# Kernel optimization log

Measured on AMD Instinct MI355X. Metric: run time of the kernel, lower is better.

The kernel has to match this reference:

```python
import jax, jax.numpy as jnp
import numpy as np

B, N, D_IN, D_OUT = 8, 2048, 512, 512


def setup_inputs() -> dict:
    key = jax.random.key(0)
    ks = jax.random.split(key, 9)
    s = 1.0 / np.sqrt(D_IN)
    return {
        "x": jax.random.normal(ks[0], (B, N, D_IN), dtype=jnp.float32),
        "adj": jax.random.uniform(ks[1], (B, N, N), dtype=jnp.float32, maxval=3.0),
        "Wq": jax.random.uniform(ks[2], (D_IN, D_OUT), jnp.float32, -s, s),
        "bq": jax.random.uniform(ks[3], (D_OUT,), jnp.float32, -s, s),
        "Wk": jax.random.uniform(ks[4], (D_IN, D_OUT), jnp.float32, -s, s),
        "bk": jax.random.uniform(ks[5], (D_OUT,), jnp.float32, -s, s),
        "Wv": jax.random.uniform(ks[6], (D_IN, D_OUT), jnp.float32, -s, s),
        "bv": jax.random.uniform(ks[7], (D_OUT,), jnp.float32, -s, s),
        "scale": jnp.float32(1.0),
        "width": jnp.float32(2.0),
    }


def reference(x, adj, Wq, bq, Wk, bk, Wv, bv, scale, width):
    # Linear projections
    Q = jnp.einsum("bnd,de->bne", x, Wq) + bq
    K = jnp.einsum("bnd,de->bne", x, Wk) + bk
    V = jnp.einsum("bnd,de->bne", x, Wv) + bv
    inv_sqrt_d = 1.0 / jnp.sqrt(jnp.float32(D_OUT))
    scores = jnp.einsum("bqe,bke->bqk", Q, K) * inv_sqrt_d  # [B,N,N]
    # Learned Gaussian distance mask, multiplicatively fused into scores
    masks = jnp.exp(-((adj - scale) ** 2 / width))
    attn = jax.nn.softmax(scores * masks, axis=-1)
    return jnp.einsum("bqk,bke->bqe", attn, V)
```

## Files before the change

### kernel.cpp

```cpp
#include <hip/hip_runtime.h>
#include <hip/hip_bf16.h>
#include <cstdint>

typedef __attribute__((ext_vector_type(4))) float f32x4;
typedef __attribute__((ext_vector_type(8))) short s16x8;

#define LOG2E 1.44269504088896340736f

#define WAITV0 asm volatile("s_waitcnt vmcnt(0)" ::: "memory")
#define WAITV2 asm volatile("s_waitcnt vmcnt(2)" ::: "memory")
#define WAITV18 asm volatile("s_waitcnt vmcnt(18)" ::: "memory")
#define WAITLG asm volatile("s_waitcnt lgkmcnt(0)" ::: "memory")
#define COMPILER_FENCE asm volatile("" ::: "memory")

__device__ __forceinline__ unsigned short f2bf(float f) {
    unsigned int u = __builtin_bit_cast(unsigned int, f);
    u += 0x7FFFu + ((u >> 16) & 1u);
    return (unsigned short)(u >> 16);
}
__device__ __forceinline__ float bf2f(unsigned short u) {
    return __builtin_bit_cast(float, (unsigned int)u << 16);
}
__device__ __forceinline__ void gload_lds16(const void* g, void* l) {
    __builtin_amdgcn_global_load_lds(
        (const __attribute__((address_space(1))) unsigned int*)g,
        (__attribute__((address_space(3))) unsigned int*)l, 16, 0, 0);
}
__device__ __forceinline__ int m3(int v) {
    if (v >= 9) v -= 9;
    if (v >= 6) v -= 6;
    if (v >= 3) v -= 3;
    return v;
}


__global__ void convert_x_kernel(const float* __restrict__ x,
                                 unsigned short* __restrict__ xb, int n4) {
    int i = blockIdx.x * blockDim.x + threadIdx.x;
    if (i < n4) {
        const float4 v = reinterpret_cast<const float4*>(x)[i];
        ushort4 o;
        o.x = f2bf(v.x); o.y = f2bf(v.y); o.z = f2bf(v.z); o.w = f2bf(v.w);
        reinterpret_cast<ushort4*>(xb)[i] = o;
    }
}

__global__ void transpose_w_kernel(const float* __restrict__ Wq,
                                   const float* __restrict__ Wk,
                                   const float* __restrict__ Wv,
                                   unsigned short* __restrict__ WT) {
    int i = blockIdx.x * blockDim.x + threadIdx.x;
    int m = i >> 18;
    int r = i & 262143;
    int n = r & 511;
    int k = r >> 9;
    const float* W = (m == 0) ? Wq : (m == 1) ? Wk : Wv;
    WT[(m << 18) + n * 512 + k] = f2bf(W[k * 512 + n]);
}

__global__ __launch_bounds__(256, 2) void proj_gemm_kernel(
    const unsigned short* __restrict__ xb,
    const unsigned short* __restrict__ WT,
    const float* __restrict__ bq, const float* __restrict__ bk, const float* __restrict__ bv,
    unsigned short* __restrict__ Qb, unsigned short* __restrict__ Kb,
    unsigned short* __restrict__ VT)
{
    const int z = blockIdx.z;
    const unsigned short* Wt = WT + (z << 18);
    const float* bias = (z == 0) ? bq : (z == 1) ? bk : bv;

    const int gm = blockIdx.x * 128;
    const int gn = blockIdx.y * 128;
    const int wave = threadIdx.x >> 6, lane = threadIdx.x & 63;
    const int wr = wave >> 1, wc = wave & 1;
    const int lr = lane & 15, lg = lane >> 4;
    const int row0 = gm + wr * 64;
    const int col0 = gn + wc * 64;

    f32x4 acc[4][4];
    #pragma unroll
    for (int mi = 0; mi < 4; mi++)
        #pragma unroll
        for (int ni = 0; ni < 4; ni++)
            acc[mi][ni] = (f32x4){0.f, 0.f, 0.f, 0.f};

    for (int k0 = 0; k0 < 512; k0 += 32) {
        s16x8 a[4], b[4];
        #pragma unroll
        for (int mi = 0; mi < 4; mi++)
            a[mi] = *reinterpret_cast<const s16x8*>(xb + (size_t)(row0 + mi * 16 + lr) * 512 + k0 + lg * 8);
        #pragma unroll
        for (int ni = 0; ni < 4; ni++)
            b[ni] = *reinterpret_cast<const s16x8*>(Wt + (size_t)(col0 + ni * 16 + lr) * 512 + k0 + lg * 8);
        #pragma unroll
        for (int mi = 0; mi < 4; mi++)
            #pragma unroll
            for (int ni = 0; ni < 4; ni++)
                acc[mi][ni] = __builtin_amdgcn_mfma_f32_16x16x32_bf16(a[mi], b[ni], acc[mi][ni], 0, 0, 0);
    }

    #pragma unroll
    for (int ni = 0; ni < 4; ni++) {
        const int col = col0 + ni * 16 + lr;
        const float bs = bias[col];
        #pragma unroll
        for (int mi = 0; mi < 4; mi++) {
            const int rowb = row0 + mi * 16 + lg * 4;
            if (z == 2) {
                unsigned short h[4];
                #pragma unroll
                for (int j = 0; j < 4; j++) h[j] = f2bf(acc[mi][ni][j] + bs);
                const int bb = rowb >> 11;
                const int nn = rowb & 2047;
                ushort4 o; o.x = h[0]; o.y = h[1]; o.z = h[2]; o.w = h[3];
                *reinterpret_cast<ushort4*>(VT + (size_t)bb * (512 * 2048) + (size_t)col * 2048 + nn) = o;
            } else {
                unsigned short* dst = (z == 0) ? Qb : Kb;
                #pragma unroll
                for (int j = 0; j < 4; j++)
                    dst[(size_t)(rowb + j) * 512 + col] = f2bf(acc[mi][ni][j] + bs);
            }
        }
    }
}

__global__ __launch_bounds__(512, 2) void attn_kernel(
    const unsigned short* __restrict__ Qb,
    const unsigned short* __restrict__ Kb,
    const unsigned short* __restrict__ VTb,
    const float* __restrict__ adj,
    const float* __restrict__ scale_p, const float* __restrict__ width_p,
    unsigned short* __restrict__ Op,
    float* __restrict__ Mp, float* __restrict__ Lp)
{
    const int bid = blockIdx.x;
    const int x8 = bid & 7, jj = bid >> 3;
    const int bk = x8 + 8 * (jj >> 5);
    const int qt = jj & 31;
    const int b    = bk >> 1;
    const int kvh  = bk & 1;
    const int wave = threadIdx.x >> 6;
    const int lane = threadIdx.x & 63;
    const int lr   = lane & 15;
    const int lg   = lane >> 4;

    __shared__ __align__(16) char smem[68096];
    char* kring = smem;
    char* vring = smem + 24576;
    unsigned short (*pbuf)[4][16][72] = (unsigned short (*)[4][16][72])(smem + 49152);
    float* corrbuf = (float*)(smem + 67584);

    if (wave < 4) {
        const int sw = wave;
        const int q0 = qt * 64 + sw * 16;
        const unsigned short* Qrow = Qb + ((size_t)b * 2048 + q0) * 512;
        const char* Kg = (const char*)Kb + ((size_t)b * 2048 + (size_t)kvh * 1024) * 1024;
        const float* adj_b = adj + (size_t)b * 2048 * 2048
                           + (size_t)(q0 + lg * 4) * 2048 + (size_t)kvh * 1024 + lr;
        const float scl = *scale_p;
        const float nw  = -LOG2E / (*width_p);
        const float cf  = 0.044194173824159216f * LOG2E;

        auto stage_k = [&](int slot, int c) {
            char* dstb = kring + slot * 8192;
            const int kvt = (c >> 3) * 64;
            const int dcb = (c & 7) * 128;
            #pragma unroll
            for (int i = 0; i < 2; i++) {
                const int sl  = sw * 2 + i;
                const int row = sl * 8 + (lane >> 3);
                const int colb = (lane & 7) * 16;
                gload_lds16(Kg + (size_t)(kvt + row) * 1024 + dcb + (colb ^ ((row & 7) << 4)),
                            dstb + sl * 1024);
            }
        };

        s16x8 qf[16];
        #pragma unroll
        for (int ks = 0; ks < 16; ks++)
            qf[ks] = __builtin_nontemporal_load(
                reinterpret_cast<const s16x8*>(Qrow + (size_t)lr * 512 + ks * 32 + lg * 8));

        f32x4 sacc[4];
        #pragma unroll
        for (int nt = 0; nt < 4; nt++) sacc[nt] = (f32x4){0.f, 0.f, 0.f, 0.f};
        float m_[4] = {-1e30f, -1e30f, -1e30f, -1e30f};
        float l_[4] = {0.f, 0.f, 0.f, 0.f};

        stage_k(0, 0);
        stage_k(1, 1);
        WAITV0;
        __builtin_amdgcn_s_barrier();

        int rcur = 0;
        for (int t = 0; t < 16; ++t) {
            const int kv0 = t * 64;
            float av[4][4];
            #pragma unroll
            for (int p = 0; p < 8; ++p) {
                const bool do_stage = (t < 15) || (p < 6);
                if (do_stage) stage_k(m3(rcur + p + 2), t * 8 + p + 2);

                if (p == 0) {
                    COMPILER_FENCE;
                    #pragma unroll
                    for (int nt = 0; nt < 4; nt++)
                        #pragma unroll
                        for (int j = 0; j < 4; j++)
                            av[nt][j] = __builtin_nontemporal_load(
                                &adj_b[(size_t)j * 2048 + kv0 + nt * 16]);
                    COMPILER_FENCE;
                }

                const char* kb_ = kring + m3(rcur + p) * 8192;
                __builtin_amdgcn_s_setprio(1);
                #pragma unroll
                for (int ks = 0; ks < 2; ks++) {
                    const s16x8 a = qf[p * 2 + ks];
                    #pragma unroll
                    for (int nt = 0; nt < 4; nt++) {
                        const int row = nt * 16 + lr;
                        const int cbyte = ks * 64 + lg * 16;
                        const s16x8 kf = *reinterpret_cast<const s16x8*>(
                            kb_ + row * 128 + (cbyte ^ ((row & 7) << 4)));
                        sacc[nt] = __builtin_amdgcn_mfma_f32_16x16x32_bf16(a, kf, sacc[nt], 0, 0, 0);
                    }
                }
                __builtin_amdgcn_s_setprio(0);

                if (p == 7) {
                    #pragma unroll
                    for (int nt = 0; nt < 4; nt++)
                        #pragma unroll
                        for (int j = 0; j < 4; j++) {
                            const float d = av[nt][j] - scl;
                            sacc[nt][j] = sacc[nt][j] * cf * exp2f(d * d * nw);
                        }
                    float corr[4];
                    #pragma unroll
                    for (int j = 0; j < 4; j++) {
                        float v = fmaxf(fmaxf(sacc[0][j], sacc[1][j]), fmaxf(sacc[2][j], sacc[3][j]));
                        #pragma unroll
                        for (int sh = 1; sh < 16; sh <<= 1) v = fmaxf(v, __shfl_xor(v, sh, 64));
                        const float mn = fmaxf(m_[j], v);
                        corr[j] = exp2f(m_[j] - mn);
                        m_[j] = mn;
                    }
                    #pragma unroll
                    for (int j = 0; j < 4; j++) {
                        float rs = 0.f;
                        #pragma unroll
                        for (int nt = 0; nt < 4; nt++) {
                            const float pv = exp2f(sacc[nt][j] - m_[j]);
                            pbuf[t & 1][sw][lg * 4 + j][nt * 16 + lr] = f2bf(pv);
                            rs += pv;
                        }
                        #pragma unroll
                        for (int sh = 1; sh < 16; sh <<= 1) rs += __shfl_xor(rs, sh, 64);
                        l_[j] = l_[j] * corr[j] + rs;
                    }
                    if (lr == 0) {
                        #pragma unroll
                        for (int j = 0; j < 4; j++)
                            corrbuf[(t & 1) * 64 + sw * 16 + lg * 4 + j] = corr[j];
                    }
                    #pragma unroll
                    for (int nt = 0; nt < 4; nt++) sacc[nt] = (f32x4){0.f, 0.f, 0.f, 0.f};
                    WAITLG;
                }
                if (p == 0 || p == 1) { WAITV18; }
                else if (do_stage)    { WAITV2; }
                else                  { WAITV0; }
                __builtin_amdgcn_s_barrier();
            }
            rcur += 2; if (rcur >= 3) rcur -= 3;
        }
        #pragma unroll
        for (int p = 0; p < 8; ++p) {
            WAITV0;
            __builtin_amdgcn_s_barrier();
        }
        const size_t prow0 = (size_t)kvh * 16384 + (size_t)b * 2048 + q0;
        if (lr == 0) {
            #pragma unroll
            for (int j = 0; j < 4; j++) {
                Mp[prow0 + lg * 4 + j] = m_[j];
                Lp[prow0 + lg * 4 + j] = l_[j];
            }
        }
    } else {
        const int ow = wave - 4;
        const int q0 = qt * 64 + ow * 16;
        const char* Vg = (const char*)VTb + ((size_t)b * 512 * 2048 + (size_t)kvh * 1024) * 2;

        auto stage_v = [&](int slot, int c) {
            char* dstb = vring + slot * 8192;
            const int kvt = (c >> 3) * 64;
            const int dr0 = (c & 7) * 64;
            #pragma unroll
            for (int i = 0; i < 2; i++) {
                const int sl  = ow * 2 + i;
                const int row = sl * 8 + (lane >> 3);
                const int colb = (lane & 7) * 16;
                gload_lds16(Vg + (size_t)(dr0 + row) * 4096 + (size_t)kvt * 2 + (colb ^ ((row & 7) << 4)),
                            dstb + sl * 1024);
            }
        };

        f32x4 oacc[32];
        #pragma unroll
        for (int i = 0; i < 32; i++) oacc[i] = (f32x4){0.f, 0.f, 0.f, 0.f};
        s16x8 pa0{}, pa1{};

        __builtin_amdgcn_s_barrier();

        #pragma unroll
        for (int p = 0; p < 8; ++p) {
            if (p == 6) stage_v(0, 0);
            if (p == 7) stage_v(1, 1);
            WAITV2;
            __builtin_amdgcn_s_barrier();
        }

        int rcur = 2;
        for (int t = 1; t < 17; ++t) {
            #pragma unroll
            for (int p = 0; p < 8; ++p) {
                const bool do_stage = (t < 16) || (p < 6);
                if (do_stage) stage_v(m3(rcur + p), t * 8 + p - 6);

                if (p == 0) {
                    const float* cl = corrbuf + ((t - 1) & 1) * 64 + ow * 16;
                    float c_[4];
                    #pragma unroll
                    for (int j = 0; j < 4; j++) c_[j] = cl[lg * 4 + j];
                    const unsigned short* pb = &pbuf[(t - 1) & 1][ow][0][0];
                    pa0 = *reinterpret_cast<const s16x8*>(pb + lr * 72 + lg * 8);
                    pa1 = *reinterpret_cast<const s16x8*>(pb + lr * 72 + 32 + lg * 8);
                    const bool need = __any(c_[0] < 1.f || c_[1] < 1.f || c_[2] < 1.f || c_[3] < 1.f);
                    if (need) {
                        #pragma unroll
                        for (int f = 0; f < 32; f++)
                            #pragma unroll
                            for (int j = 0; j < 4; j++) oacc[f][j] *= c_[j];
                    }
                }

                const char* vb_ = vring + m3(rcur + p + 1) * 8192;
                __builtin_amdgcn_s_setprio(1);
                #pragma unroll
                for (int ks2 = 0; ks2 < 2; ks2++) {
                    const s16x8 pa = (ks2 == 0) ? pa0 : pa1;
                    #pragma unroll
                    for (int df2 = 0; df2 < 4; df2++) {
                        const int row = df2 * 16 + lr;
                        const int cbyte = ks2 * 64 + lg * 16;
                        const s16x8 vf = *reinterpret_cast<const s16x8*>(
                            vb_ + row * 128 + (cbyte ^ ((row & 7) << 4)));
                        oacc[p * 4 + df2] = __builtin_amdgcn_mfma_f32_16x16x32_bf16(pa, vf, oacc[p * 4 + df2], 0, 0, 0);
                    }
                }
                __builtin_amdgcn_s_setprio(0);

                if (do_stage) { WAITV2; } else { WAITV0; }
                __builtin_amdgcn_s_barrier();
            }
            rcur += 2; if (rcur >= 3) rcur -= 3;
        }

        unsigned short* lds_t = (unsigned short*)smem + (size_t)ow * 4224;
        const size_t prow0 = (size_t)kvh * 16384 + (size_t)b * 2048 + q0;
        #pragma unroll
        for (int h = 0; h < 2; ++h) {
            #pragma unroll
            for (int dd = 0; dd < 16; ++dd) {
                const int df = h * 16 + dd;
                #pragma unroll
                for (int j = 0; j < 4; ++j)
                    lds_t[(lg * 4 + j) * 264 + dd * 16 + lr] = f2bf(oacc[df][j]);
            }
            #pragma unroll
            for (int g2 = 0; g2 < 2; ++g2) {
                const int r16  = g2 * 8 + (lane >> 3);
                const int colu = (lane & 7) * 8;
                unsigned short* oprow = Op + (prow0 + r16) * 512 + h * 256;
                #pragma unroll
                for (int k = 0; k < 4; ++k) {
                    const s16x8 v = *reinterpret_cast<const s16x8*>(&lds_t[r16 * 264 + colu + k * 64]);
                    __builtin_nontemporal_store(v, reinterpret_cast<s16x8*>(oprow + colu + k * 64));
                }
            }
        }
    }
}

__global__ void combine_kernel(const unsigned short* __restrict__ Op,
                               const float* __restrict__ Mp, const float* __restrict__ Lp,
                               float* __restrict__ out) {
    const int idx = blockIdx.x * 256 + threadIdx.x;
    const int r   = idx >> 6;
    const int c8  = (idx & 63) * 8;
    const float m0 = Mp[r], m1 = Mp[16384 + r];
    const float l0 = Lp[r], l1 = Lp[16384 + r];
    const float M  = fmaxf(m0, m1);
    const float e0 = exp2f(m0 - M), e1 = exp2f(m1 - M);
    const float invL = 1.f / (e0 * l0 + e1 * l1);
    const s16x8 a = __builtin_nontemporal_load(
        reinterpret_cast<const s16x8*>(Op + (size_t)r * 512 + c8));
    const s16x8 bq = __builtin_nontemporal_load(
        reinterpret_cast<const s16x8*>(Op + (size_t)16384 * 512 + (size_t)r * 512 + c8));
    float o[8];
    #pragma unroll
    for (int i = 0; i < 8; i++)
        o[i] = (bf2f((unsigned short)a[i]) * e0 + bf2f((unsigned short)bq[i]) * e1) * invL;
    f32x4* dst = reinterpret_cast<f32x4*>(out + (size_t)r * 512 + c8);
    __builtin_nontemporal_store((f32x4){o[0], o[1], o[2], o[3]}, dst);
    __builtin_nontemporal_store((f32x4){o[4], o[5], o[6], o[7]}, dst + 1);
}


extern "C" void kernel_launch(void* const* d_in, const int* in_sizes, int n_in,
                              void* d_out, int out_size, void* d_ws, size_t ws_size,
                              hipStream_t stream) {
    const float* x     = (const float*)d_in[0];
    const float* adj   = (const float*)d_in[1];
    const float* Wq    = (const float*)d_in[2];
    const float* bq    = (const float*)d_in[3];
    const float* Wk    = (const float*)d_in[4];
    const float* bk    = (const float*)d_in[5];
    const float* Wv    = (const float*)d_in[6];
    const float* bv    = (const float*)d_in[7];
    const float* scale = (const float*)d_in[8];
    const float* width = (const float*)d_in[9];

    char* ws = (char*)d_ws;
    unsigned short* xb = (unsigned short*)(ws);
    unsigned short* WT = (unsigned short*)(ws + 16777216);
    unsigned short* Qb = (unsigned short*)(ws + 18350080);
    unsigned short* Kb = (unsigned short*)(ws + 35127296);
    unsigned short* VT = (unsigned short*)(ws + 51904512);
    unsigned short* Op = (unsigned short*)(ws + 68681728);
    float*          Mp = (float*)(ws + 102236160);
    float*          Lp = (float*)(ws + 102367232);
    float* out = (float*)d_out;

    hipLaunchKernelGGL(convert_x_kernel, dim3(8192), dim3(256), 0, stream, x, xb, 8388608 / 4);
    hipLaunchKernelGGL(transpose_w_kernel, dim3(3072), dim3(256), 0, stream, Wq, Wk, Wv, WT);
    hipLaunchKernelGGL(proj_gemm_kernel, dim3(128, 4, 3), dim3(256), 0, stream,
                       xb, WT, bq, bk, bv, Qb, Kb, VT);
    hipLaunchKernelGGL(attn_kernel, dim3(512), dim3(512), 0, stream,
                       Qb, Kb, VT, adj, scale, width, Op, Mp, Lp);
    hipLaunchKernelGGL(combine_kernel, dim3(4096), dim3(256), 0, stream, Op, Mp, Lp, out);
}
```

Measured before the change: 285.6 us.

## Read K directly from global in score waves and widen V staging chunks

New measurement: 474.1 us. +66.0%, slower.

```diff
diff --git a/kernel.cpp b/kernel.cpp
--- a/kernel.cpp
+++ b/kernel.cpp
@@ -8,10 +8,8 @@
 #define LOG2E 1.44269504088896340736f
 
 #define WAITV0 asm volatile("s_waitcnt vmcnt(0)" ::: "memory")
-#define WAITV2 asm volatile("s_waitcnt vmcnt(2)" ::: "memory")
-#define WAITV18 asm volatile("s_waitcnt vmcnt(18)" ::: "memory")
+#define WAITV4 asm volatile("s_waitcnt vmcnt(4)" ::: "memory")
 #define WAITLG asm volatile("s_waitcnt lgkmcnt(0)" ::: "memory")
-#define COMPILER_FENCE asm volatile("" ::: "memory")
 
 __device__ __forceinline__ unsigned short f2bf(float f) {
     unsigned int u = __builtin_bit_cast(unsigned int, f);
@@ -25,12 +23,6 @@
     __builtin_amdgcn_global_load_lds(
         (const __attribute__((address_space(1))) unsigned int*)g,
         (__attribute__((address_space(3))) unsigned int*)l, 16, 0, 0);
-}
-__device__ __forceinline__ int m3(int v) {
-    if (v >= 9) v -= 9;
-    if (v >= 6) v -= 6;
-    if (v >= 3) v -= 3;
-    return v;
 }
 
 
@@ -145,8 +137,7 @@
     const int lg   = lane >> 4;
 
     __shared__ __align__(16) char smem[68096];
-    char* kring = smem;
-    char* vring = smem + 24576;
+    char* vring = smem;
     unsigned short (*pbuf)[4][16][72] = (unsigned short (*)[4][16][72])(smem + 49152);
     float* corrbuf = (float*)(smem + 67584);
 
@@ -161,20 +152,6 @@
         const float nw  = -LOG2E / (*width_p);
         const float cf  = 0.044194173824159216f * LOG2E;
 
-        auto stage_k = [&](int slot, int c) {
-            char* dstb = kring + slot * 8192;
-            const int kvt = (c >> 3) * 64;
-            const int dcb = (c & 7) * 128;
-            #pragma unroll
-            for (int i = 0; i < 2; i++) {
-                const int sl  = sw * 2 + i;
-                const int row = sl * 8 + (lane >> 3);
-                const int colb = (lane & 7) * 16;
-                gload_lds16(Kg + (size_t)(kvt + row) * 1024 + dcb + (colb ^ ((row & 7) << 4)),
-                            dstb + sl * 1024);
-            }
-        };
-
         s16x8 qf[16];
         #pragma unroll
         for (int ks = 0; ks < 16; ks++)
@@ -187,48 +164,37 @@
         float m_[4] = {-1e30f, -1e30f, -1e30f, -1e30f};
         float l_[4] = {0.f, 0.f, 0.f, 0.f};
 
-        stage_k(0, 0);
-        stage_k(1, 1);
-        WAITV0;
         __builtin_amdgcn_s_barrier();
 
-        int rcur = 0;
         for (int t = 0; t < 16; ++t) {
             const int kv0 = t * 64;
             float av[4][4];
             #pragma unroll
-            for (int p = 0; p < 8; ++p) {
-                const bool do_stage = (t < 15) || (p < 6);
-                if (do_stage) stage_k(m3(rcur + p + 2), t * 8 + p + 2);
-
+            for (int p = 0; p < 4; ++p) {
                 if (p == 0) {
-                    COMPILER_FENCE;
                     #pragma unroll
                     for (int nt = 0; nt < 4; nt++)
                         #pragma unroll
                         for (int j = 0; j < 4; j++)
                             av[nt][j] = __builtin_nontemporal_load(
                                 &adj_b[(size_t)j * 2048 + kv0 + nt * 16]);
-                    COMPILER_FENCE;
-                }
-
-                const char* kb_ = kring + m3(rcur + p) * 8192;
+                }
+
                 __builtin_amdgcn_s_setprio(1);
                 #pragma unroll
-                for (int ks = 0; ks < 2; ks++) {
-                    const s16x8 a = qf[p * 2 + ks];
+                for (int ks = 0; ks < 4; ks++) {
+                    const int idx = p * 4 + ks;
+                    const s16x8 a = qf[idx];
                     #pragma unroll
                     for (int nt = 0; nt < 4; nt++) {
-                        const int row = nt * 16 + lr;
-                        const int cbyte = ks * 64 + lg * 16;
                         const s16x8 kf = *reinterpret_cast<const s16x8*>(
-                            kb_ + row * 128 + (cbyte ^ ((row & 7) << 4)));
+                            Kg + (size_t)(kv0 + nt * 16 + lr) * 1024 + idx * 64 + lg * 16);
                         sacc[nt] = __builtin_amdgcn_mfma_f32_16x16x32_bf16(a, kf, sacc[nt], 0, 0, 0);
                     }
                 }
                 __builtin_amdgcn_s_setprio(0);
 
-                if (p == 7) {
+                if (p == 3) {
                     #pragma unroll
                     for (int nt = 0; nt < 4; nt++)
                         #pragma unroll
@@ -268,15 +234,11 @@
                     for (int nt = 0; nt < 4; nt++) sacc[nt] = (f32x4){0.f, 0.f, 0.f, 0.f};
                     WAITLG;
                 }
-                if (p == 0 || p == 1) { WAITV18; }
-                else if (do_stage)    { WAITV2; }
-                else                  { WAITV0; }
                 __builtin_amdgcn_s_barrier();
             }
-            rcur += 2; if (rcur >= 3) rcur -= 3;
-        }
-        #pragma unroll
-        for (int p = 0; p < 8; ++p) {
+        }
+        #pragma unroll
+        for (int p = 0; p < 4; ++p) {
             WAITV0;
             __builtin_amdgcn_s_barrier();
         }
@@ -294,12 +256,12 @@
         const char* Vg = (const char*)VTb + ((size_t)b * 512 * 2048 + (size_t)kvh * 1024) * 2;
 
         auto stage_v = [&](int slot, int c) {
-            char* dstb = vring + slot * 8192;
-            const int kvt = (c >> 3) * 64;
-            const int dr0 = (c & 7) * 64;
-            #pragma unroll
-            for (int i = 0; i < 2; i++) {
-                const int sl  = ow * 2 + i;
+            char* dstb = vring + slot * 16384;
+            const int kvt = (c >> 2) * 64;
+            const int dr0 = (c & 3) * 128;
+            #pragma unroll
+            for (int i = 0; i < 4; i++) {
+                const int sl  = ow * 4 + i;
                 const int row = sl * 8 + (lane >> 3);
                 const int colb = (lane & 7) * 16;
                 gload_lds16(Vg + (size_t)(dr0 + row) * 4096 + (size_t)kvt * 2 + (colb ^ ((row & 7) << 4)),
@@ -315,19 +277,21 @@
         __builtin_amdgcn_s_barrier();
 
         #pragma unroll
-        for (int p = 0; p < 8; ++p) {
-            if (p == 6) stage_v(0, 0);
-            if (p == 7) stage_v(1, 1);
-            WAITV2;
+        for (int p = 0; p < 4; ++p) {
+            if (p == 2) stage_v(1, 0);
+            if (p == 3) stage_v(2, 1);
+            WAITV4;
             __builtin_amdgcn_s_barrier();
         }
 
-        int rcur = 2;
+        int ss = 0;
+        int cs = 1;
         for (int t = 1; t < 17; ++t) {
             #pragma unroll
-            for (int p = 0; p < 8; ++p) {
-                const bool do_stage = (t < 16) || (p < 6);
-                if (do_stage) stage_v(m3(rcur + p), t * 8 + p - 6);
+            for (int p = 0; p < 4; ++p) {
+                const int c_s = t * 4 + p - 2;
+                const bool do_stage = (c_s <= 63);
+                if (do_stage) { stage_v(ss, c_s); ss = (ss == 2) ? 0 : ss + 1; }
 
                 if (p == 0) {
                     const float* cl = corrbuf + ((t - 1) & 1) * 64 + ow * 16;
@@ -346,26 +310,26 @@
                     }
                 }
 
-                const char* vb_ = vring + m3(rcur + p + 1) * 8192;
+                const char* vb_ = vring + cs * 16384;
+                cs = (cs == 2) ? 0 : cs + 1;
                 __builtin_amdgcn_s_setprio(1);
                 #pragma unroll
                 for (int ks2 = 0; ks2 < 2; ks2++) {
                     const s16x8 pa = (ks2 == 0) ? pa0 : pa1;
                     #pragma unroll
-                    for (int df2 = 0; df2 < 4; df2++) {
+                    for (int df2 = 0; df2 < 8; df2++) {
                         const int row = df2 * 16 + lr;
                         const int cbyte = ks2 * 64 + lg * 16;
                         const s16x8 vf = *reinterpret_cast<const s16x8*>(
                             vb_ + row * 128 + (cbyte ^ ((row & 7) << 4)));
-                        oacc[p * 4 + df2] = __builtin_amdgcn_mfma_f32_16x16x32_bf16(pa, vf, oacc[p * 4 + df2], 0, 0, 0);
+                        oacc[p * 8 + df2] = __builtin_amdgcn_mfma_f32_16x16x32_bf16(pa, vf, oacc[p * 8 + df2], 0, 0, 0);
                     }
                 }
                 __builtin_amdgcn_s_setprio(0);
 
-                if (do_stage) { WAITV2; } else { WAITV0; }
+                if (do_stage) { WAITV4; } else { WAITV0; }
                 __builtin_amdgcn_s_barrier();
             }
-            rcur += 2; if (rcur >= 3) rcur -= 3;
         }
 
         unsigned short* lds_t = (unsigned short*)smem + (size_t)ow * 4224;
```
